# Kernel tuning notes

Hardware: AMD Instinct MI355X
Metric: run time of the kernel (lower is better)

Reference implementation:

```python
import jax, jax.numpy as jnp
import numpy as np

B, S, D = 4, 2048, 768
H = 12
HD = D // H
SCALE = HD ** -0.5


def setup_inputs() -> dict:
    key = jax.random.key(0)
    ks = jax.random.split(key, 5)
    std = D ** -0.5
    return {
        "hidden_states": jax.random.normal(ks[0], (B, S, D), dtype=jnp.float32),
        "qkv_w": jax.random.normal(ks[1], (3 * D, D), dtype=jnp.float32) * std,
        "qkv_b": jnp.zeros((3 * D,), dtype=jnp.float32),
        "proj_w": jax.random.normal(ks[2], (D, D), dtype=jnp.float32) * std,
        "proj_b": jnp.zeros((D,), dtype=jnp.float32),
    }


def reference(hidden_states, qkv_w, qkv_b, proj_w, proj_b):
    b, s, d = hidden_states.shape
    # fused QKV projection: [b,s,3d] -> [3,b,H,s,hd]
    mixed = hidden_states @ qkv_w.T + qkv_b
    mixed = mixed.reshape(b, s, 3, H, HD).transpose(2, 0, 3, 1, 4)
    q, k, v = mixed[0], mixed[1], mixed[2]
    # naive attention: full [b,H,s,s] score matrix, as in original module
    scores = jnp.einsum("bhqd,bhkd->bhqk", q, k) * SCALE
    probs = jax.nn.softmax(scores, axis=-1)
    ctx = jnp.einsum("bhqk,bhkd->bhqd", probs, v)
    ctx = ctx.transpose(0, 2, 1, 3).reshape(b, s, d)
    out = ctx @ proj_w.T + proj_b
    return out
```

## Files before the change

kernel.cpp:

```cpp
#include <hip/hip_runtime.h>
#include <hip/hip_bf16.h>

using short8   = __attribute__((ext_vector_type(8))) short;
using floatx4  = __attribute__((ext_vector_type(4))) float;
using floatx16 = __attribute__((ext_vector_type(16))) float;

#define KDIM 768
#define QSCALE 0.18033688011112042f
#define N1 (8192 * 768)
#define N2 (2304 * 768)
#define N3 (768 * 768)

__device__ __forceinline__ short f2bf(float f) {
    union { float f; unsigned u; } v; v.f = f;
    unsigned r = v.u + 0x7fffu + ((v.u >> 16) & 1u);
    return (short)(r >> 16);
}

__device__ __forceinline__ unsigned pack2bf(float a, float b) {
    __hip_bfloat162 h = __float22bfloat162_rn(float2{a, b});
    union { __hip_bfloat162 h; unsigned u; } c; c.h = h;
    return c.u;
}

__device__ __forceinline__ float fast_exp2(float x) {
#if __has_builtin(__builtin_amdgcn_exp2f)
    return __builtin_amdgcn_exp2f(x);
#else
    return exp2f(x);
#endif
}

__device__ __forceinline__ void async16(const void* g, void* l) {
    __builtin_amdgcn_global_load_lds((const __attribute__((address_space(1))) void*)g,
                                     (__attribute__((address_space(3))) void*)l, 16, 0, 0);
}

__global__ void cvt_all(const float* __restrict__ a, const float* __restrict__ b,
                        const float* __restrict__ c, short* __restrict__ oa,
                        short* __restrict__ ob, short* __restrict__ oc) {
    int i = (blockIdx.x * blockDim.x + threadIdx.x) * 4;
    const float* src; short* dst;
    if (i < N1)            { src = a + i;            dst = oa + i; }
    else if (i < N1 + N2)  { src = b + (i - N1);     dst = ob + (i - N1); }
    else if (i < N1+N2+N3) { src = c + (i - N1 - N2); dst = oc + (i - N1 - N2); }
    else return;
    float4 v = *(const float4*)src;
    short4 o;
    o.x = f2bf(v.x); o.y = f2bf(v.y); o.z = f2bf(v.z); o.w = f2bf(v.w);
    *(short4*)dst = o;
}

__global__ __launch_bounds__(256) void gemm_qkv(
    const short* __restrict__ X, const short* __restrict__ W,
    const float* __restrict__ bias,
    short* __restrict__ Qb, short* __restrict__ Kb, short* __restrict__ Vb)
{
    __shared__ short Smem[128 * 144];
    short* As = Smem;
    short* Bs = Smem + 128 * 32;
    int tid = threadIdx.x;
    int w = tid >> 6, l = tid & 63;
    int lane16 = l & 15, quad = l >> 4;
    int wm = w & 1, wn = w >> 1;

    int fid = blockIdx.x + 18 * blockIdx.y;
    int c = fid & 7, s = fid >> 3;
    int my = c * 8 + s / 18;
    int nx = s % 18;
    int m0 = my * 128, n0 = nx * 128;

    floatx4 acc[4][4] = {};

    int srow = w * 32 + (l >> 2);
    int scol = (l & 3) * 8;
    const short* Xg = X + (size_t)(m0 + srow) * KDIM + scol;
    const short* Wg = W + (size_t)(n0 + srow) * KDIM + scol;
    short* AsW = As + (w * 32) * 32;
    short* BsW = Bs + (w * 32) * 32;

    for (int kb = 0; kb < KDIM; kb += 32) {
        __syncthreads();
        async16(Xg + kb,              AsW);
        async16(Xg + kb + 16 * KDIM,  AsW + 16 * 32);
        async16(Wg + kb,              BsW);
        async16(Wg + kb + 16 * KDIM,  BsW + 16 * 32);
        __syncthreads();
        short8 a[4], b[4];
#pragma unroll
        for (int mt = 0; mt < 4; mt++) a[mt] = *(const short8*)(As + (wm * 64 + mt * 16 + lane16) * 32 + quad * 8);
#pragma unroll
        for (int nt = 0; nt < 4; nt++) b[nt] = *(const short8*)(Bs + (wn * 64 + nt * 16 + lane16) * 32 + quad * 8);
#pragma unroll
        for (int mt = 0; mt < 4; mt++)
#pragma unroll
            for (int nt = 0; nt < 4; nt++)
                acc[mt][nt] = __builtin_amdgcn_mfma_f32_16x16x32_bf16(a[mt], b[nt], acc[mt][nt], 0, 0, 0);
    }

    int qkv = nx / 6;
    float sc = (qkv == 0) ? (float)QSCALE : 1.0f;
    short* dst = (qkv == 0) ? Qb : ((qkv == 1) ? Kb : Vb);
    int h0 = (nx - qkv * 6) * 2;
    int b_ = m0 >> 11, s0 = m0 & 2047;

    __syncthreads();
#pragma unroll
    for (int mt = 0; mt < 4; mt++) {
        int rowl = wm * 64 + mt * 16 + quad * 4;
#pragma unroll
        for (int nt = 0; nt < 4; nt++) {
            int coll = wn * 64 + nt * 16 + lane16;
            float bv = bias[n0 + coll];
#pragma unroll
            for (int r = 0; r < 4; r++)
                Smem[(rowl + r) * 144 + coll] = f2bf((acc[mt][nt][r] + bv) * sc);
        }
    }
    __syncthreads();
#pragma unroll
    for (int i = 0; i < 8; i++) {
        int slot = i * 256 + tid;
        int ch = slot >> 10;
        int rem2 = slot & 1023;
        int s_loc = rem2 >> 3, e8 = rem2 & 7;
        short8 v = *(const short8*)(Smem + s_loc * 144 + ch * 64 + e8 * 8);
        *(short8*)(dst + (((size_t)(b_ * 12 + h0 + ch)) * 2048 + s0 + s_loc) * 64 + e8 * 8) = v;
    }
}

__global__ __launch_bounds__(256) void transpose_v(
    const short* __restrict__ Vb, short* __restrict__ Vt)
{
    __shared__ short T[64 * 66];
    int tid = threadIdx.x;
    int s0 = blockIdx.x * 64, bh = blockIdx.y;
    const short* src = Vb + (size_t)bh * 2048 * 64;
    short* dst = Vt + (size_t)bh * 64 * 2048;

#pragma unroll
    for (int i = 0; i < 2; i++) {
        int slot = i * 256 + tid;
        int s_loc = slot >> 3, ec = slot & 7;
        short8 v = *(const short8*)(src + (size_t)(s0 + s_loc) * 64 + ec * 8);
        *(short8*)(T + s_loc * 66 + ec * 8) = v;
    }
    __syncthreads();
#pragma unroll
    for (int i = 0; i < 2; i++) {
        int slot = i * 256 + tid;
        int e_loc = slot >> 3, sc = slot & 7;
        short8 o;
#pragma unroll
        for (int j = 0; j < 8; j++) {
            int p = sc * 8 + j;
            int kp = (p & 0x33) | ((p & 4) << 1) | ((p & 8) >> 1);
            o[j] = T[kp * 66 + e_loc];
        }
        *(short8*)(dst + (size_t)e_loc * 2048 + s0 + sc * 8) = o;
    }
}

__global__ __launch_bounds__(256, 3) void attn(
    const short* __restrict__ Qb, const short* __restrict__ Kb,
    const short* __restrict__ Vt, short* __restrict__ Ctx)
{
    __shared__ short Ks[3][512 * 8];
    __shared__ short Vs[3][512 * 8];
    int tid = threadIdx.x, w = tid >> 6, l = tid & 63;
    int l32 = l & 31, half = l >> 5;

    int fid = blockIdx.x + (blockIdx.y << 4);
    int c = fid & 7, sfl = fid >> 3;
    int bh = c * 6 + (sfl >> 4);
    int qt = sfl & 15;

    const short* Qh  = Qb + (size_t)bh * 2048 * 64;
    const short* Kh  = Kb + (size_t)bh * 2048 * 64;
    const short* Vth = Vt + (size_t)bh * 64 * 2048;
    int qbase = qt * 128 + w * 32;

    const short* kSrc[2];
    const short* vSrc[2];
    int dOff[2];
#pragma unroll
    for (int i = 0; i < 2; i++) {
        int slot = i * 256 + tid;
        int row = slot >> 3;
        int g = (slot & 7) ^ (row & 7);
        kSrc[i] = Kh + (size_t)row * 64 + g * 8;
        vSrc[i] = Vth + (size_t)row * 2048 + g * 8;
        dOff[i] = (i * 256 + w * 64) * 8;
    }

    short8 qf[4];
#pragma unroll
    for (int ks = 0; ks < 4; ks++)
        qf[ks] = *(const short8*)(Qh + (size_t)(qbase + l32) * 64 + ks * 16 + half * 8);

#pragma unroll
    for (int i = 0; i < 2; i++) {
        async16(kSrc[i],                  &Ks[0][0] + dOff[i]);
        async16(vSrc[i],                  &Vs[0][0] + dOff[i]);
    }
#pragma unroll
    for (int i = 0; i < 2; i++) {
        async16(kSrc[i] + 4096,           &Ks[1][0] + dOff[i]);
        async16(vSrc[i] + 64,             &Vs[1][0] + dOff[i]);
    }

    float lsum = 0.f;
    floatx16 acc[2] = {};
    int sw = l32 & 7;

    int cur = 0;
    for (int kt = 0; kt < 32; kt++) {
        if (kt < 31) { asm volatile("s_waitcnt vmcnt(4)" ::: "memory"); }
        else         { asm volatile("s_waitcnt vmcnt(0)" ::: "memory"); }
        __builtin_amdgcn_s_barrier();

        int pf = kt + 2;
        if (pf < 32) {
            int pb = cur >= 1 ? cur - 1 : cur + 2;
#pragma unroll
            for (int i = 0; i < 2; i++) {
                async16(kSrc[i] + (size_t)pf * 4096, &Ks[pb][0] + dOff[i]);
                async16(vSrc[i] + (size_t)pf * 64,   &Vs[pb][0] + dOff[i]);
            }
        }

        const short* Kcur = &Ks[cur][0];
        const short* Vcur = &Vs[cur][0];

        floatx16 s[2];
        __builtin_amdgcn_s_setprio(1);
#pragma unroll
        for (int nt = 0; nt < 2; nt++) {
            floatx16 cacc = {};
            int rowb = (nt * 32 + l32) * 8;
#pragma unroll
            for (int ks = 0; ks < 4; ks++) {
                short8 kf = *(const short8*)(Kcur + (size_t)(rowb + ((ks * 2 + half) ^ sw)) * 8);
                cacc = __builtin_amdgcn_mfma_f32_32x32x16_bf16(kf, qf[ks], cacc, 0, 0, 0);
            }
            s[nt] = cacc;
        }
        __builtin_amdgcn_s_setprio(0);

        union { short8 s8; unsigned u[4]; } pa[4];
#pragma unroll
        for (int nt = 0; nt < 2; nt++)
#pragma unroll
            for (int r = 0; r < 16; r += 2) {
                float p0 = fast_exp2(s[nt][r]);
                float p1 = fast_exp2(s[nt][r + 1]);
                lsum += p0 + p1;
                pa[2 * nt + (r >> 3)].u[(r & 7) >> 1] = pack2bf(p0, p1);
            }

        __builtin_amdgcn_s_setprio(1);
#pragma unroll
        for (int nt = 0; nt < 2; nt++) {
            int rowb = (nt * 32 + l32) * 8;
#pragma unroll
            for (int ks = 0; ks < 4; ks++) {
                short8 vf = *(const short8*)(Vcur + (size_t)(rowb + ((ks * 2 + half) ^ sw)) * 8);
                acc[nt] = __builtin_amdgcn_mfma_f32_32x32x16_bf16(pa[ks].s8, vf, acc[nt], 0, 0, 0);
            }
        }
        __builtin_amdgcn_s_setprio(0);

        cur = (cur == 2) ? 0 : cur + 1;
    }

    float denom = lsum + __shfl_xor(lsum, 32);
    float inv_self = 1.0f / denom;

    int b_ = bh / 12, h = bh % 12;
#pragma unroll
    for (int nt = 0; nt < 2; nt++)
#pragma unroll
        for (int r = 0; r < 16; r++) {
            int qloc = (r & 3) + 8 * (r >> 2) + 4 * half;
            float invq = __shfl(inv_self, qloc);
            int q = qbase + qloc;
            int e = nt * 32 + l32;
            Ctx[((size_t)(b_ * 2048 + q)) * 768 + h * 64 + e] = f2bf(acc[nt][r] * invq);
        }
}

__global__ __launch_bounds__(256) void gemm_out(
    const short* __restrict__ Ctx, const short* __restrict__ W,
    const float* __restrict__ bias, float* __restrict__ out)
{
    __shared__ short As[64 * 32];
    __shared__ short Bs[128 * 32];
    int tid = threadIdx.x;
    int w = tid >> 6, l = tid & 63;
    int lane16 = l & 15, quad = l >> 4;
    int wm = w & 1, wn = w >> 1;

    int fid = blockIdx.x + 6 * blockIdx.y;
    int c = fid & 7, s = fid >> 3;
    int my = c * 16 + s / 6;
    int nx = s % 6;
    int m0 = my * 64, n0 = nx * 128;

    floatx4 acc[2][4] = {};

    int srow = tid >> 2;
    int scol = (tid & 3) * 8;
    const short* Xg = Ctx + (size_t)(m0 + srow) * KDIM + scol;
    const short* Wg = W + (size_t)(n0 + srow) * KDIM + scol;
    short* AsW = As + (w * 16) * 32;
    short* BsW = Bs + (w * 16) * 32;

    for (int kb = 0; kb < KDIM; kb += 32) {
        __syncthreads();
        async16(Xg + kb,             AsW);
        async16(Wg + kb,             BsW);
        async16(Wg + kb + 64 * KDIM, BsW + 64 * 32);
        __syncthreads();
        short8 a[2], b[4];
#pragma unroll
        for (int mt = 0; mt < 2; mt++) a[mt] = *(const short8*)(As + (wm * 32 + mt * 16 + lane16) * 32 + quad * 8);
#pragma unroll
        for (int nt = 0; nt < 4; nt++) b[nt] = *(const short8*)(Bs + (wn * 64 + nt * 16 + lane16) * 32 + quad * 8);
#pragma unroll
        for (int mt = 0; mt < 2; mt++)
#pragma unroll
            for (int nt = 0; nt < 4; nt++)
                acc[mt][nt] = __builtin_amdgcn_mfma_f32_16x16x32_bf16(a[mt], b[nt], acc[mt][nt], 0, 0, 0);
    }

#pragma unroll
    for (int mt = 0; mt < 2; mt++) {
        int row = m0 + wm * 32 + mt * 16 + quad * 4;
#pragma unroll
        for (int nt = 0; nt < 4; nt++) {
            int col = n0 + wn * 64 + nt * 16 + lane16;
            float bv = bias[col];
#pragma unroll
            for (int r = 0; r < 4; r++)
                out[(size_t)(row + r) * 768 + col] = acc[mt][nt][r] + bv;
        }
    }
}

extern "C" void kernel_launch(void* const* d_in, const int* in_sizes, int n_in,
                              void* d_out, int out_size, void* d_ws, size_t ws_size,
                              hipStream_t stream) {
    const float* hs     = (const float*)d_in[0];
    const float* qkv_w  = (const float*)d_in[1];
    const float* qkv_b  = (const float*)d_in[2];
    const float* proj_w = (const float*)d_in[3];
    const float* proj_b = (const float*)d_in[4];
    float* out = (float*)d_out;

    short* Xb  = (short*)d_ws;
    short* W1b = Xb  + (size_t)8192 * 768;
    short* W2b = W1b + (size_t)2304 * 768;
    short* Qb  = W2b + (size_t)768 * 768;
    short* Kb  = Qb  + (size_t)8192 * 768;
    short* Vb  = Kb  + (size_t)8192 * 768;
    short* Ctx = Vb  + (size_t)8192 * 768;
    short* Vt  = Xb;

    int ntot = (N1 + N2 + N3) / 4;
    cvt_all<<<(ntot + 255) / 256, 256, 0, stream>>>(hs, qkv_w, proj_w, Xb, W1b, W2b);

    gemm_qkv<<<dim3(18, 64), 256, 0, stream>>>(Xb, W1b, qkv_b, Qb, Kb, Vb);
    transpose_v<<<dim3(32, 48), 256, 0, stream>>>(Vb, Vt);
    attn<<<dim3(16, 48), 256, 0, stream>>>(Qb, Kb, Vt, Ctx);
    gemm_out<<<dim3(6, 128), 256, 0, stream>>>(Ctx, W2b, proj_b, out);
}
```

Before: 218.6 us.

## Widen GEMM K-step to 64 with XOR-swizzled LDS and reorder QKV tile mapping

```diff
diff --git a/kernel.cpp b/kernel.cpp
--- a/kernel.cpp
+++ b/kernel.cpp
@@ -58,7 +58,7 @@
 {
     __shared__ short Smem[128 * 144];
     short* As = Smem;
-    short* Bs = Smem + 128 * 32;
+    short* Bs = Smem + 128 * 64;
     int tid = threadIdx.x;
     int w = tid >> 6, l = tid & 63;
     int lane16 = l & 15, quad = l >> 4;
@@ -66,36 +66,41 @@
 
     int fid = blockIdx.x + 18 * blockIdx.y;
     int c = fid & 7, s = fid >> 3;
-    int my = c * 8 + s / 18;
-    int nx = s % 18;
+    int nx = s >> 3;
+    int my = c * 8 + (s & 7);
     int m0 = my * 128, n0 = nx * 128;
 
     floatx4 acc[4][4] = {};
 
-    int srow = w * 32 + (l >> 2);
-    int scol = (l & 3) * 8;
-    const short* Xg = X + (size_t)(m0 + srow) * KDIM + scol;
-    const short* Wg = W + (size_t)(n0 + srow) * KDIM + scol;
-    short* AsW = As + (w * 32) * 32;
-    short* BsW = Bs + (w * 32) * 32;
-
-    for (int kb = 0; kb < KDIM; kb += 32) {
+    int srow = 8 * w + (l >> 3);
+    int g = ((l & 7) ^ (l >> 3)) * 8;
+    const short* Xg = X + (size_t)(m0 + srow) * KDIM + g;
+    const short* Wg = W + (size_t)(n0 + srow) * KDIM + g;
+    int swr = lane16 & 7;
+
+    for (int kb = 0; kb < KDIM; kb += 64) {
         __syncthreads();
-        async16(Xg + kb,              AsW);
-        async16(Xg + kb + 16 * KDIM,  AsW + 16 * 32);
-        async16(Wg + kb,              BsW);
-        async16(Wg + kb + 16 * KDIM,  BsW + 16 * 32);
+#pragma unroll
+        for (int j = 0; j < 4; j++) {
+            async16(Xg + (size_t)j * 32 * KDIM + kb, As + (j * 32 + 8 * w) * 64);
+            async16(Wg + (size_t)j * 32 * KDIM + kb, Bs + (j * 32 + 8 * w) * 64);
+        }
         __syncthreads();
-        short8 a[4], b[4];
-#pragma unroll
-        for (int mt = 0; mt < 4; mt++) a[mt] = *(const short8*)(As + (wm * 64 + mt * 16 + lane16) * 32 + quad * 8);
-#pragma unroll
-        for (int nt = 0; nt < 4; nt++) b[nt] = *(const short8*)(Bs + (wn * 64 + nt * 16 + lane16) * 32 + quad * 8);
-#pragma unroll
-        for (int mt = 0; mt < 4; mt++)
+#pragma unroll
+        for (int ks = 0; ks < 2; ks++) {
+            short8 a[4], b[4];
+#pragma unroll
+            for (int mt = 0; mt < 4; mt++)
+                a[mt] = *(const short8*)(As + (wm * 64 + mt * 16 + lane16) * 64 + ((ks * 4 + quad) ^ swr) * 8);
 #pragma unroll
             for (int nt = 0; nt < 4; nt++)
-                acc[mt][nt] = __builtin_amdgcn_mfma_f32_16x16x32_bf16(a[mt], b[nt], acc[mt][nt], 0, 0, 0);
+                b[nt] = *(const short8*)(Bs + (wn * 64 + nt * 16 + lane16) * 64 + ((ks * 4 + quad) ^ swr) * 8);
+#pragma unroll
+            for (int mt = 0; mt < 4; mt++)
+#pragma unroll
+                for (int nt = 0; nt < 4; nt++)
+                    acc[mt][nt] = __builtin_amdgcn_mfma_f32_16x16x32_bf16(a[mt], b[nt], acc[mt][nt], 0, 0, 0);
+        }
     }
 
     int qkv = nx / 6;
@@ -200,13 +205,13 @@
 
 #pragma unroll
     for (int i = 0; i < 2; i++) {
-        async16(kSrc[i],                  &Ks[0][0] + dOff[i]);
-        async16(vSrc[i],                  &Vs[0][0] + dOff[i]);
-    }
-#pragma unroll
-    for (int i = 0; i < 2; i++) {
-        async16(kSrc[i] + 4096,           &Ks[1][0] + dOff[i]);
-        async16(vSrc[i] + 64,             &Vs[1][0] + dOff[i]);
+        async16(kSrc[i],        &Ks[0][0] + dOff[i]);
+        async16(vSrc[i],        &Vs[0][0] + dOff[i]);
+    }
+#pragma unroll
+    for (int i = 0; i < 2; i++) {
+        async16(kSrc[i] + 4096, &Ks[1][0] + dOff[i]);
+        async16(vSrc[i] + 64,   &Vs[1][0] + dOff[i]);
     }
 
     float lsum = 0.f;
@@ -293,8 +298,8 @@
     const short* __restrict__ Ctx, const short* __restrict__ W,
     const float* __restrict__ bias, float* __restrict__ out)
 {
-    __shared__ short As[64 * 32];
-    __shared__ short Bs[128 * 32];
+    __shared__ short As[64 * 64];
+    __shared__ short Bs[128 * 64];
     int tid = threadIdx.x;
     int w = tid >> 6, l = tid & 63;
     int lane16 = l & 15, quad = l >> 4;
@@ -308,29 +313,36 @@
 
     floatx4 acc[2][4] = {};
 
-    int srow = tid >> 2;
-    int scol = (tid & 3) * 8;
-    const short* Xg = Ctx + (size_t)(m0 + srow) * KDIM + scol;
-    const short* Wg = W + (size_t)(n0 + srow) * KDIM + scol;
-    short* AsW = As + (w * 16) * 32;
-    short* BsW = Bs + (w * 16) * 32;
-
-    for (int kb = 0; kb < KDIM; kb += 32) {
+    int srow = 8 * w + (l >> 3);
+    int g = ((l & 7) ^ (l >> 3)) * 8;
+    const short* Xg = Ctx + (size_t)(m0 + srow) * KDIM + g;
+    const short* Wg = W + (size_t)(n0 + srow) * KDIM + g;
+    int swr = lane16 & 7;
+
+    for (int kb = 0; kb < KDIM; kb += 64) {
         __syncthreads();
-        async16(Xg + kb,             AsW);
-        async16(Wg + kb,             BsW);
-        async16(Wg + kb + 64 * KDIM, BsW + 64 * 32);
+#pragma unroll
+        for (int j = 0; j < 2; j++)
+            async16(Xg + (size_t)j * 32 * KDIM + kb, As + (j * 32 + 8 * w) * 64);
+#pragma unroll
+        for (int j = 0; j < 4; j++)
+            async16(Wg + (size_t)j * 32 * KDIM + kb, Bs + (j * 32 + 8 * w) * 64);
         __syncthreads();
-        short8 a[2], b[4];
-#pragma unroll
-        for (int mt = 0; mt < 2; mt++) a[mt] = *(const short8*)(As + (wm * 32 + mt * 16 + lane16) * 32 + quad * 8);
-#pragma unroll
-        for (int nt = 0; nt < 4; nt++) b[nt] = *(const short8*)(Bs + (wn * 64 + nt * 16 + lane16) * 32 + quad * 8);
-#pragma unroll
-        for (int mt = 0; mt < 2; mt++)
+#pragma unroll
+        for (int ks = 0; ks < 2; ks++) {
+            short8 a[2], b[4];
+#pragma unroll
+            for (int mt = 0; mt < 2; mt++)
+                a[mt] = *(const short8*)(As + (wm * 32 + mt * 16 + lane16) * 64 + ((ks * 4 + quad) ^ swr) * 8);
 #pragma unroll
             for (int nt = 0; nt < 4; nt++)
-                acc[mt][nt] = __builtin_amdgcn_mfma_f32_16x16x32_bf16(a[mt], b[nt], acc[mt][nt], 0, 0, 0);
+                b[nt] = *(const short8*)(Bs + (wn * 64 + nt * 16 + lane16) * 64 + ((ks * 4 + quad) ^ swr) * 8);
+#pragma unroll
+            for (int mt = 0; mt < 2; mt++)
+#pragma unroll
+                for (int nt = 0; nt < 4; nt++)
+                    acc[mt][nt] = __builtin_amdgcn_mfma_f32_16x16x32_bf16(a[mt], b[nt], acc[mt][nt], 0, 0, 0);
+        }
     }
 
 #pragma unroll
```

Measured after the change: 223.8 us. +2.4%, slower.
